# Performance work log

Hardware: AMD Instinct MI355X
Metric: run time of the kernel (lower is better)

Reference implementation:

```python
import jax, jax.numpy as jnp
import numpy as np

E = 600000
N = 50000
H = 128
OE = 256


def swish(v):
    return v * jax.nn.sigmoid(v)


def setup_inputs() -> dict:
    key = jax.random.key(0)
    ks = jax.random.split(key, 16)
    inp = {
        "x": jax.random.normal(ks[0], (E, H), dtype=jnp.float32),
        "rbf": jax.random.normal(ks[1], (E, 6), dtype=jnp.float32),
        "i": jax.random.randint(ks[2], (E,), 0, N, dtype=jnp.int32),
        "edge_index": jax.random.randint(ks[3], (2, E), 0, N, dtype=jnp.int32),
        "edge_weight": jax.random.uniform(ks[4], (E,), dtype=jnp.float32),
        "batch": jax.random.randint(ks[5], (N,), 0, 32, dtype=jnp.int32),
        "num_nodes": N,
        "W_rbf": jax.random.normal(ks[6], (H, 6), dtype=jnp.float32) * 0.2,
        "W_up": jax.random.normal(ks[7], (OE, H), dtype=jnp.float32) * (1.0 / np.sqrt(H)),
        "b_up": jnp.zeros((OE,), dtype=jnp.float32),
        "W_l1": jax.random.normal(ks[8], (OE, OE), dtype=jnp.float32) * (1.0 / np.sqrt(OE)),
        "b_l1": jnp.zeros((OE,), dtype=jnp.float32),
        "W_l2": jax.random.normal(ks[9], (OE, OE), dtype=jnp.float32) * (1.0 / np.sqrt(OE)),
        "b_l2": jnp.zeros((OE,), dtype=jnp.float32),
        "W_l3": jax.random.normal(ks[10], (OE, OE), dtype=jnp.float32) * (1.0 / np.sqrt(OE)),
        "b_l3": jnp.zeros((OE,), dtype=jnp.float32),
        "W_out": jax.random.normal(ks[11], (1, OE), dtype=jnp.float32) * (1.0 / np.sqrt(OE)),
        "W_w": jax.random.normal(ks[12], (1, H), dtype=jnp.float32) * (1.0 / np.sqrt(H)),
        "b_w": jnp.zeros((1,), dtype=jnp.float32),
    }
    return inp


def reference(x, rbf, i, edge_index, edge_weight, batch, num_nodes,
              W_rbf, W_up, b_up, W_l1, b_l1, W_l2, b_l2, W_l3, b_l3,
              W_out, W_w, b_w):
    # edge_index / edge_weight are unused in the original forward.
    # x = lin_rbf(rbf) * x  -> [E, H]
    xe = (rbf @ W_rbf.T) * x
    # scatter-add edges -> nodes: [N, H]
    xn = jax.ops.segment_sum(xe, i, num_segments=num_nodes)
    # energy head: alpha = w_lin(x) before lin_up
    alpha = xn @ W_w.T + b_w  # [N, 1]
    x2 = xn @ W_up.T + b_up   # [N, OE]
    for W, b in ((W_l1, b_l1), (W_l2, b_l2), (W_l3, b_l3)):
        x2 = swish(x2 @ W.T + b)
    out = (x2 @ W_out.T) * alpha  # [N, 1]
    return (out, batch)
```

## Files before the change

kernel.cpp:

```cpp
#include <hip/hip_runtime.h>
#include <hip/hip_bf16.h>
#include <math.h>

#define E_CNT 600000
#define N_CNT 50000
#define H_DIM 128
#define OE_DIM 256

typedef __attribute__((ext_vector_type(8))) short short8;
typedef __attribute__((ext_vector_type(4))) float f32x4;

#define WS_EIDS   0
#define WS_OFF    2400000
#define WS_CURS   2600008
#define WS_CNT    2800008
#define WS_WUP    3000016
#define WS_WL1    3065552
#define WS_WL2    3196624
#define WS_WL3    3327696
#define WS_TEXC   3500000
#define WS_BSUM   3700704
#define WS_BEXC   3701728

#define SCAN_NB 196
#define WCONV_NB 896

__global__ __launch_bounds__(256) void histwconv_kernel(
    const int* __restrict__ nid, int* __restrict__ counts,
    const float* __restrict__ Wup, const float* __restrict__ Wl1,
    const float* __restrict__ Wl2, const float* __restrict__ Wl3,
    ushort* __restrict__ dUp, ushort* __restrict__ dL1,
    ushort* __restrict__ dL2, ushort* __restrict__ dL3)
{
    if (blockIdx.x < WCONV_NB) {
        int d = blockIdx.x * 256 + threadIdx.x;
        const float* W;
        ushort* dst;
        int K;
        if (d < 32768)       { W = Wup; dst = dUp; K = 128; }
        else if (d < 98304)  { d -= 32768;  W = Wl1; dst = dL1; K = 256; }
        else if (d < 163840) { d -= 98304;  W = Wl2; dst = dL2; K = 256; }
        else                 { d -= 163840; W = Wl3; dst = dL3; K = 256; }
        int j = d & 7;
        int l = (d >> 3) & 63;
        int KS = K >> 5;
        int ks = (d >> 9) % KS;
        int ot = (d >> 9) / KS;
        int k = ks * 32 + ((l >> 4) << 3) + j;
        int o = ot * 16 + (l & 15);
        __hip_bfloat16 h = __float2bfloat16(W[o * K + k]);
        dst[d] = *(const ushort*)&h;
    } else {
        int nb = gridDim.x - WCONV_NB;
        for (int e = (blockIdx.x - WCONV_NB) * 256 + threadIdx.x; e < E_CNT;
             e += nb * 256)
            atomicAdd(&counts[nid[e]], 1);
    }
}

__global__ __launch_bounds__(256) void scanA_kernel(const int* __restrict__ counts,
                                                    int* __restrict__ texc,
                                                    int* __restrict__ bsum)
{
    __shared__ int s[256];
    const int t = threadIdx.x;
    const int i = blockIdx.x * 256 + t;
    int v = (i < N_CNT) ? counts[i] : 0;
    s[t] = v;
    __syncthreads();
    for (int off = 1; off < 256; off <<= 1) {
        int u = (t >= off) ? s[t - off] : 0;
        __syncthreads();
        s[t] += u;
        __syncthreads();
    }
    texc[i] = s[t] - v;
    if (t == 255) bsum[blockIdx.x] = s[255];
}

__global__ __launch_bounds__(256) void scanB_kernel(const int* __restrict__ bsum,
                                                    int* __restrict__ bexc)
{
    __shared__ int s[256];
    const int t = threadIdx.x;
    int v = (t < SCAN_NB) ? bsum[t] : 0;
    s[t] = v;
    __syncthreads();
    for (int off = 1; off < 256; off <<= 1) {
        int u = (t >= off) ? s[t - off] : 0;
        __syncthreads();
        s[t] += u;
        __syncthreads();
    }
    bexc[t] = s[t] - v;
}

__global__ __launch_bounds__(256) void scanC_kernel(const int* __restrict__ texc,
                                                    const int* __restrict__ bexc,
                                                    int* __restrict__ offs,
                                                    int* __restrict__ cursor)
{
    const int i = blockIdx.x * 256 + threadIdx.x;
    if (i < N_CNT) {
        int o = texc[i] + bexc[i >> 8];
        offs[i] = o;
        cursor[i] = o;
    }
    if (i == 0) offs[N_CNT] = E_CNT;
}

__global__ __launch_bounds__(256) void fill_kernel(const int* __restrict__ nid,
                                                   int* __restrict__ cursor,
                                                   int* __restrict__ eids)
{
    for (int e = blockIdx.x * 256 + threadIdx.x; e < E_CNT; e += gridDim.x * 256) {
        int slot = atomicAdd(&cursor[nid[e]], 1);
        eids[slot] = e;
    }
}

#define MB 64
#define PITCH 264
#define EMAX 2048

template<int KS, bool SW>
__device__ __forceinline__ void layer(const ushort* __restrict__ Wsh,
                                      const float* __restrict__ bias,
                                      const ushort* in_s, ushort* out_s, int tid)
{
    const int w = tid >> 6, lane = tid & 63;
    const int l15 = lane & 15, lg = lane >> 4;

    f32x4 acc[4][2];
#pragma unroll
    for (int mi = 0; mi < 4; ++mi)
#pragma unroll
        for (int oi = 0; oi < 2; ++oi)
            acc[mi][oi] = (f32x4){0.f, 0.f, 0.f, 0.f};

#pragma unroll
    for (int ks = 0; ks < KS; ++ks) {
        short8 b[2];
#pragma unroll
        for (int oi = 0; oi < 2; ++oi)
            b[oi] = *(const short8*)(Wsh + (size_t)(((w * 2 + oi) * KS + ks) * 64 + lane) * 8);
#pragma unroll
        for (int mi = 0; mi < 4; ++mi) {
            short8 a = *(const short8*)(in_s + (mi * 16 + l15) * PITCH + ks * 32 + lg * 8);
#pragma unroll
            for (int oi = 0; oi < 2; ++oi)
                acc[mi][oi] = __builtin_amdgcn_mfma_f32_16x16x32_bf16(a, b[oi], acc[mi][oi], 0, 0, 0);
        }
    }

#pragma unroll
    for (int oi = 0; oi < 2; ++oi) {
        float bv = bias[(w * 2 + oi) * 16 + l15];
#pragma unroll
        for (int mi = 0; mi < 4; ++mi)
#pragma unroll
            for (int r = 0; r < 4; ++r) {
                float v = acc[mi][oi][r] + bv;
                if (SW) v = v / (1.f + __expf(-v));
                __hip_bfloat16 h = __float2bfloat16(v);
                out_s[(mi * 16 + lg * 4 + r) * PITCH + (w * 2 + oi) * 16 + l15] =
                    *(const ushort*)&h;
            }
    }
}

__global__ __launch_bounds__(512, 4) void fused_kernel(
    const float* __restrict__ x, const float* __restrict__ rbf,
    const int* __restrict__ offs, const int* __restrict__ eids,
    const float* __restrict__ W_rbf, const float* __restrict__ W_w,
    const float* __restrict__ b_w,
    const ushort* __restrict__ Wup, const ushort* __restrict__ Wl1,
    const ushort* __restrict__ Wl2, const ushort* __restrict__ Wl3,
    const float* __restrict__ b_up, const float* __restrict__ b_l1,
    const float* __restrict__ b_l2, const float* __restrict__ b_l3,
    const float* __restrict__ W_out, const int* __restrict__ batch,
    float* __restrict__ out)
{
    __shared__ ushort sA[MB * PITCH];
    __shared__ ushort sB[MB * PITCH];
    __shared__ float s_alpha[MB];
    __shared__ int s_eids[EMAX];

    const int tid = threadIdx.x;
    const int w = tid >> 6, lane = tid & 63;
    const int node0 = blockIdx.x * MB;

    if (tid < MB) {
        int node = node0 + tid;
        if (node < N_CNT) out[N_CNT + node] = (float)batch[node];
    }

    const int nend = min(node0 + MB, N_CNT);
    const int s0 = offs[node0];
    const int tot = offs[nend] - s0;
    const bool staged = (tot <= EMAX);
    if (staged)
        for (int t = tid; t < tot; t += 512) s_eids[t] = eids[s0 + t];
    const int* ep = staged ? (const int*)s_eids : (eids + s0);
    __syncthreads();

    {
        const int half = lane >> 5;
        const int hb = (lane & 31) * 4;
        float wrb[4][6];
#pragma unroll
        for (int j = 0; j < 4; ++j)
#pragma unroll
            for (int k = 0; k < 6; ++k)
                wrb[j][k] = W_rbf[(hb + j) * 6 + k];
        float ww[4];
#pragma unroll
        for (int j = 0; j < 4; ++j) ww[j] = W_w[hb + j];

        for (int nl8 = 0; nl8 < 8; ++nl8) {
            const int nl = w * 8 + nl8;
            const int node = node0 + nl;
            int ls = 0, le = 0;
            if (node < N_CNT) {
                ls = offs[node] - s0;
                le = offs[node + 1] - s0;
            }
            float a0 = 0.f, a1 = 0.f, a2 = 0.f, a3 = 0.f;
            int i = ls;
            for (; i + 1 < le; i += 2) {
                const int ee = ep[i + half];
                const float4 xv = *(const float4*)(x + (size_t)ee * H_DIM + hb);
                float r[6];
#pragma unroll
                for (int k = 0; k < 6; ++k) r[k] = rbf[ee * 6 + k];
                float c0 = 0.f, c1 = 0.f, c2 = 0.f, c3 = 0.f;
#pragma unroll
                for (int k = 0; k < 6; ++k) {
                    c0 = fmaf(r[k], wrb[0][k], c0);
                    c1 = fmaf(r[k], wrb[1][k], c1);
                    c2 = fmaf(r[k], wrb[2][k], c2);
                    c3 = fmaf(r[k], wrb[3][k], c3);
                }
                a0 = fmaf(c0, xv.x, a0);
                a1 = fmaf(c1, xv.y, a1);
                a2 = fmaf(c2, xv.z, a2);
                a3 = fmaf(c3, xv.w, a3);
            }
            if (i < le && half == 0) {
                const int ee = ep[i];
                const float4 xv = *(const float4*)(x + (size_t)ee * H_DIM + hb);
                float r[6];
#pragma unroll
                for (int k = 0; k < 6; ++k) r[k] = rbf[ee * 6 + k];
                float c0 = 0.f, c1 = 0.f, c2 = 0.f, c3 = 0.f;
#pragma unroll
                for (int k = 0; k < 6; ++k) {
                    c0 = fmaf(r[k], wrb[0][k], c0);
                    c1 = fmaf(r[k], wrb[1][k], c1);
                    c2 = fmaf(r[k], wrb[2][k], c2);
                    c3 = fmaf(r[k], wrb[3][k], c3);
                }
                a0 = fmaf(c0, xv.x, a0);
                a1 = fmaf(c1, xv.y, a1);
                a2 = fmaf(c2, xv.z, a2);
                a3 = fmaf(c3, xv.w, a3);
            }

            a0 += __shfl_xor(a0, 32);
            a1 += __shfl_xor(a1, 32);
            a2 += __shfl_xor(a2, 32);
            a3 += __shfl_xor(a3, 32);

            if (half == 0) {
                __hip_bfloat16 h0 = __float2bfloat16(a0), h1 = __float2bfloat16(a1);
                __hip_bfloat16 h2 = __float2bfloat16(a2), h3 = __float2bfloat16(a3);
                ushort4 pk;
                pk.x = *(const ushort*)&h0;
                pk.y = *(const ushort*)&h1;
                pk.z = *(const ushort*)&h2;
                pk.w = *(const ushort*)&h3;
                *(ushort4*)(sA + nl * PITCH + hb) = pk;
            }

            float part = fmaf(a0, ww[0], fmaf(a1, ww[1], fmaf(a2, ww[2], a3 * ww[3])));
            part += __shfl_xor(part, 1);
            part += __shfl_xor(part, 2);
            part += __shfl_xor(part, 4);
            part += __shfl_xor(part, 8);
            part += __shfl_xor(part, 16);
            if (lane == 0) s_alpha[nl] = part + b_w[0];
        }
    }
    __syncthreads();

    layer<4, false>(Wup, b_up, sA, sB, tid);
    __syncthreads();
    layer<8, true>(Wl1, b_l1, sB, sA, tid);
    __syncthreads();
    layer<8, true>(Wl2, b_l2, sA, sB, tid);
    __syncthreads();
    layer<8, true>(Wl3, b_l3, sB, sA, tid);
    __syncthreads();

    {
        int nl = tid >> 3, q = tid & 7;
        const ushort* rowp = sA + nl * PITCH + q * 32;
        float sum = 0.f;
#pragma unroll
        for (int o = 0; o < 32; ++o) {
            __hip_bfloat16 h = *(const __hip_bfloat16*)(rowp + o);
            sum = fmaf(__bfloat162float(h), W_out[q * 32 + o], sum);
        }
        sum += __shfl_xor(sum, 1);
        sum += __shfl_xor(sum, 2);
        sum += __shfl_xor(sum, 4);
        int node = node0 + nl;
        if (q == 0 && node < N_CNT) out[node] = sum * s_alpha[nl];
    }
}

extern "C" void kernel_launch(void* const* d_in, const int* in_sizes, int n_in,
                              void* d_out, int out_size, void* d_ws, size_t ws_size,
                              hipStream_t stream)
{
    const float* x      = (const float*)d_in[0];
    const float* rbf    = (const float*)d_in[1];
    const int*   nid    = (const int*)d_in[2];
    const int*   batch  = (const int*)d_in[5];
    const float* W_rbf  = (const float*)d_in[7];
    const float* W_up   = (const float*)d_in[8];
    const float* b_up   = (const float*)d_in[9];
    const float* W_l1   = (const float*)d_in[10];
    const float* b_l1   = (const float*)d_in[11];
    const float* W_l2   = (const float*)d_in[12];
    const float* b_l2   = (const float*)d_in[13];
    const float* W_l3   = (const float*)d_in[14];
    const float* b_l3   = (const float*)d_in[15];
    const float* W_out  = (const float*)d_in[16];
    const float* W_w    = (const float*)d_in[17];
    const float* b_w    = (const float*)d_in[18];

    char* ws = (char*)d_ws;
    int*    eids   = (int*)(ws + WS_EIDS);
    int*    offs   = (int*)(ws + WS_OFF);
    int*    cursor = (int*)(ws + WS_CURS);
    int*    counts = (int*)(ws + WS_CNT);
    ushort* WupS   = (ushort*)(ws + WS_WUP);
    ushort* Wl1S   = (ushort*)(ws + WS_WL1);
    ushort* Wl2S   = (ushort*)(ws + WS_WL2);
    ushort* Wl3S   = (ushort*)(ws + WS_WL3);
    int*    texc   = (int*)(ws + WS_TEXC);
    int*    bsum   = (int*)(ws + WS_BSUM);
    int*    bexc   = (int*)(ws + WS_BEXC);
    float*  out    = (float*)d_out;

    hipMemsetAsync(counts, 0, N_CNT * sizeof(int), stream);
    histwconv_kernel<<<WCONV_NB + 1024, 256, 0, stream>>>(
        nid, counts, W_up, W_l1, W_l2, W_l3, WupS, Wl1S, Wl2S, Wl3S);
    scanA_kernel<<<SCAN_NB, 256, 0, stream>>>(counts, texc, bsum);
    scanB_kernel<<<1, 256, 0, stream>>>(bsum, bexc);
    scanC_kernel<<<SCAN_NB, 256, 0, stream>>>(texc, bexc, offs, cursor);
    fill_kernel<<<1024, 256, 0, stream>>>(nid, cursor, eids);

    fused_kernel<<<(N_CNT + MB - 1) / MB, 512, 0, stream>>>(
        x, rbf, offs, eids, W_rbf, W_w, b_w,
        WupS, Wl1S, Wl2S, Wl3S, b_up, b_l1, b_l2, b_l3, W_out, batch, out);
}
```

Measured before the change: 226.7 us.

## Single-buffer activations in LDS and raise occupancy of fused node kernel

```diff
diff --git a/kernel.cpp b/kernel.cpp
--- a/kernel.cpp
+++ b/kernel.cpp
@@ -121,12 +121,93 @@
 
 #define MB 64
 #define PITCH 264
-#define EMAX 2048
+#define EMAX 1280
+
+__device__ __forceinline__ void gather_phase(
+    const int* ep,
+    const float* __restrict__ x, const float* __restrict__ rbf,
+    const int* s_off, int s0, float bw,
+    const float (&wrb)[4][6], const float (&ww)[4],
+    ushort* act, float* s_alpha, int w, int lane)
+{
+    const int half = lane >> 5;
+    const int hb = (lane & 31) * 4;
+
+    for (int nl8 = 0; nl8 < 8; ++nl8) {
+        const int nl = w * 8 + nl8;
+        const int ls = s_off[nl] - s0;
+        const int le = s_off[nl + 1] - s0;
+        float a0 = 0.f, a1 = 0.f, a2 = 0.f, a3 = 0.f;
+        int i = ls;
+        for (; i + 1 < le; i += 2) {
+            const int ee = ep[i + half];
+            const float4 xv = *(const float4*)(x + (size_t)ee * H_DIM + hb);
+            const float2* rp = (const float2*)(rbf + (size_t)ee * 6);
+            const float2 r01 = rp[0], r23 = rp[1], r45 = rp[2];
+            float r[6] = {r01.x, r01.y, r23.x, r23.y, r45.x, r45.y};
+            float c0 = 0.f, c1 = 0.f, c2 = 0.f, c3 = 0.f;
+#pragma unroll
+            for (int k = 0; k < 6; ++k) {
+                c0 = fmaf(r[k], wrb[0][k], c0);
+                c1 = fmaf(r[k], wrb[1][k], c1);
+                c2 = fmaf(r[k], wrb[2][k], c2);
+                c3 = fmaf(r[k], wrb[3][k], c3);
+            }
+            a0 = fmaf(c0, xv.x, a0);
+            a1 = fmaf(c1, xv.y, a1);
+            a2 = fmaf(c2, xv.z, a2);
+            a3 = fmaf(c3, xv.w, a3);
+        }
+        if (i < le && half == 0) {
+            const int ee = ep[i];
+            const float4 xv = *(const float4*)(x + (size_t)ee * H_DIM + hb);
+            const float2* rp = (const float2*)(rbf + (size_t)ee * 6);
+            const float2 r01 = rp[0], r23 = rp[1], r45 = rp[2];
+            float r[6] = {r01.x, r01.y, r23.x, r23.y, r45.x, r45.y};
+            float c0 = 0.f, c1 = 0.f, c2 = 0.f, c3 = 0.f;
+#pragma unroll
+            for (int k = 0; k < 6; ++k) {
+                c0 = fmaf(r[k], wrb[0][k], c0);
+                c1 = fmaf(r[k], wrb[1][k], c1);
+                c2 = fmaf(r[k], wrb[2][k], c2);
+                c3 = fmaf(r[k], wrb[3][k], c3);
+            }
+            a0 = fmaf(c0, xv.x, a0);
+            a1 = fmaf(c1, xv.y, a1);
+            a2 = fmaf(c2, xv.z, a2);
+            a3 = fmaf(c3, xv.w, a3);
+        }
+
+        a0 += __shfl_xor(a0, 32);
+        a1 += __shfl_xor(a1, 32);
+        a2 += __shfl_xor(a2, 32);
+        a3 += __shfl_xor(a3, 32);
+
+        if (half == 0) {
+            __hip_bfloat16 h0 = __float2bfloat16(a0), h1 = __float2bfloat16(a1);
+            __hip_bfloat16 h2 = __float2bfloat16(a2), h3 = __float2bfloat16(a3);
+            ushort4 pk;
+            pk.x = *(const ushort*)&h0;
+            pk.y = *(const ushort*)&h1;
+            pk.z = *(const ushort*)&h2;
+            pk.w = *(const ushort*)&h3;
+            *(ushort4*)(act + nl * PITCH + hb) = pk;
+        }
+
+        float part = fmaf(a0, ww[0], fmaf(a1, ww[1], fmaf(a2, ww[2], a3 * ww[3])));
+        part += __shfl_xor(part, 1);
+        part += __shfl_xor(part, 2);
+        part += __shfl_xor(part, 4);
+        part += __shfl_xor(part, 8);
+        part += __shfl_xor(part, 16);
+        if (lane == 0) s_alpha[nl] = part + bw;
+    }
+}
 
 template<int KS, bool SW>
-__device__ __forceinline__ void layer(const ushort* __restrict__ Wsh,
-                                      const float* __restrict__ bias,
-                                      const ushort* in_s, ushort* out_s, int tid)
+__device__ __forceinline__ void layer_sb(const ushort* __restrict__ Wsh,
+                                         const float* __restrict__ bias,
+                                         ushort* act, int tid)
 {
     const int w = tid >> 6, lane = tid & 63;
     const int l15 = lane & 15, lg = lane >> 4;
@@ -146,12 +227,13 @@
             b[oi] = *(const short8*)(Wsh + (size_t)(((w * 2 + oi) * KS + ks) * 64 + lane) * 8);
 #pragma unroll
         for (int mi = 0; mi < 4; ++mi) {
-            short8 a = *(const short8*)(in_s + (mi * 16 + l15) * PITCH + ks * 32 + lg * 8);
+            short8 a = *(const short8*)(act + (mi * 16 + l15) * PITCH + ks * 32 + lg * 8);
 #pragma unroll
             for (int oi = 0; oi < 2; ++oi)
                 acc[mi][oi] = __builtin_amdgcn_mfma_f32_16x16x32_bf16(a, b[oi], acc[mi][oi], 0, 0, 0);
         }
     }
+    __syncthreads();
 
 #pragma unroll
     for (int oi = 0; oi < 2; ++oi) {
@@ -163,13 +245,14 @@
                 float v = acc[mi][oi][r] + bv;
                 if (SW) v = v / (1.f + __expf(-v));
                 __hip_bfloat16 h = __float2bfloat16(v);
-                out_s[(mi * 16 + lg * 4 + r) * PITCH + (w * 2 + oi) * 16 + l15] =
+                act[(mi * 16 + lg * 4 + r) * PITCH + (w * 2 + oi) * 16 + l15] =
                     *(const ushort*)&h;
             }
     }
-}
-
-__global__ __launch_bounds__(512, 4) void fused_kernel(
+    __syncthreads();
+}
+
+__global__ __launch_bounds__(512, 8) void fused_kernel(
     const float* __restrict__ x, const float* __restrict__ rbf,
     const int* __restrict__ offs, const int* __restrict__ eids,
     const float* __restrict__ W_rbf, const float* __restrict__ W_w,
@@ -181,10 +264,10 @@
     const float* __restrict__ W_out, const int* __restrict__ batch,
     float* __restrict__ out)
 {
-    __shared__ ushort sA[MB * PITCH];
-    __shared__ ushort sB[MB * PITCH];
+    __shared__ ushort act[MB * PITCH];
+    __shared__ int s_eids[EMAX];
+    __shared__ int s_off[MB + 1];
     __shared__ float s_alpha[MB];
-    __shared__ int s_eids[EMAX];
 
     const int tid = threadIdx.x;
     const int w = tid >> 6, lane = tid & 63;
@@ -194,18 +277,18 @@
         int node = node0 + tid;
         if (node < N_CNT) out[N_CNT + node] = (float)batch[node];
     }
-
-    const int nend = min(node0 + MB, N_CNT);
-    const int s0 = offs[node0];
-    const int tot = offs[nend] - s0;
+    if (tid < MB + 1)
+        s_off[tid] = offs[min(node0 + tid, N_CNT)];
+    __syncthreads();
+
+    const int s0 = s_off[0];
+    const int tot = s_off[MB] - s0;
     const bool staged = (tot <= EMAX);
     if (staged)
         for (int t = tid; t < tot; t += 512) s_eids[t] = eids[s0 + t];
-    const int* ep = staged ? (const int*)s_eids : (eids + s0);
     __syncthreads();
 
     {
-        const int half = lane >> 5;
         const int hb = (lane & 31) * 4;
         float wrb[4][6];
 #pragma unroll
@@ -216,95 +299,23 @@
         float ww[4];
 #pragma unroll
         for (int j = 0; j < 4; ++j) ww[j] = W_w[hb + j];
-
-        for (int nl8 = 0; nl8 < 8; ++nl8) {
-            const int nl = w * 8 + nl8;
-            const int node = node0 + nl;
-            int ls = 0, le = 0;
-            if (node < N_CNT) {
-                ls = offs[node] - s0;
-                le = offs[node + 1] - s0;
-            }
-            float a0 = 0.f, a1 = 0.f, a2 = 0.f, a3 = 0.f;
-            int i = ls;
-            for (; i + 1 < le; i += 2) {
-                const int ee = ep[i + half];
-                const float4 xv = *(const float4*)(x + (size_t)ee * H_DIM + hb);
-                float r[6];
-#pragma unroll
-                for (int k = 0; k < 6; ++k) r[k] = rbf[ee * 6 + k];
-                float c0 = 0.f, c1 = 0.f, c2 = 0.f, c3 = 0.f;
-#pragma unroll
-                for (int k = 0; k < 6; ++k) {
-                    c0 = fmaf(r[k], wrb[0][k], c0);
-                    c1 = fmaf(r[k], wrb[1][k], c1);
-                    c2 = fmaf(r[k], wrb[2][k], c2);
-                    c3 = fmaf(r[k], wrb[3][k], c3);
-                }
-                a0 = fmaf(c0, xv.x, a0);
-                a1 = fmaf(c1, xv.y, a1);
-                a2 = fmaf(c2, xv.z, a2);
-                a3 = fmaf(c3, xv.w, a3);
-            }
-            if (i < le && half == 0) {
-                const int ee = ep[i];
-                const float4 xv = *(const float4*)(x + (size_t)ee * H_DIM + hb);
-                float r[6];
-#pragma unroll
-                for (int k = 0; k < 6; ++k) r[k] = rbf[ee * 6 + k];
-                float c0 = 0.f, c1 = 0.f, c2 = 0.f, c3 = 0.f;
-#pragma unroll
-                for (int k = 0; k < 6; ++k) {
-                    c0 = fmaf(r[k], wrb[0][k], c0);
-                    c1 = fmaf(r[k], wrb[1][k], c1);
-                    c2 = fmaf(r[k], wrb[2][k], c2);
-                    c3 = fmaf(r[k], wrb[3][k], c3);
-                }
-                a0 = fmaf(c0, xv.x, a0);
-                a1 = fmaf(c1, xv.y, a1);
-                a2 = fmaf(c2, xv.z, a2);
-                a3 = fmaf(c3, xv.w, a3);
-            }
-
-            a0 += __shfl_xor(a0, 32);
-            a1 += __shfl_xor(a1, 32);
-            a2 += __shfl_xor(a2, 32);
-            a3 += __shfl_xor(a3, 32);
-
-            if (half == 0) {
-                __hip_bfloat16 h0 = __float2bfloat16(a0), h1 = __float2bfloat16(a1);
-                __hip_bfloat16 h2 = __float2bfloat16(a2), h3 = __float2bfloat16(a3);
-                ushort4 pk;
-                pk.x = *(const ushort*)&h0;
-                pk.y = *(const ushort*)&h1;
-                pk.z = *(const ushort*)&h2;
-                pk.w = *(const ushort*)&h3;
-                *(ushort4*)(sA + nl * PITCH + hb) = pk;
-            }
-
-            float part = fmaf(a0, ww[0], fmaf(a1, ww[1], fmaf(a2, ww[2], a3 * ww[3])));
-            part += __shfl_xor(part, 1);
-            part += __shfl_xor(part, 2);
-            part += __shfl_xor(part, 4);
-            part += __shfl_xor(part, 8);
-            part += __shfl_xor(part, 16);
-            if (lane == 0) s_alpha[nl] = part + b_w[0];
-        }
-    }
-    __syncthreads();
-
-    layer<4, false>(Wup, b_up, sA, sB, tid);
-    __syncthreads();
-    layer<8, true>(Wl1, b_l1, sB, sA, tid);
-    __syncthreads();
-    layer<8, true>(Wl2, b_l2, sA, sB, tid);
-    __syncthreads();
-    layer<8, true>(Wl3, b_l3, sB, sA, tid);
-    __syncthreads();
+        const float bw = b_w[0];
+
+        if (staged)
+            gather_phase(s_eids, x, rbf, s_off, s0, bw, wrb, ww, act, s_alpha, w, lane);
+        else
+            gather_phase(eids + s0, x, rbf, s_off, s0, bw, wrb, ww, act, s_alpha, w, lane);
+    }
+    __syncthreads();
+
+    layer_sb<4, false>(Wup, b_up, act, tid);
+    layer_sb<8, true>(Wl1, b_l1, act, tid);
+    layer_sb<8, true>(Wl2, b_l2, act, tid);
+    layer_sb<8, true>(Wl3, b_l3, act, tid);
 
     {
         int nl = tid >> 3, q = tid & 7;
-        const ushort* rowp = sA + nl * PITCH + q * 32;
+        const ushort* rowp = act + nl * PITCH + q * 32;
         float sum = 0.f;
 #pragma unroll
         for (int o = 0; o < 32; ++o) {
```

Result: slower. 255.8 us (+12.8%).

## Halve node tile to 32 and stream edge ids through chunked shared staging

Applied to the files above, without the earlier changes.

```diff
diff --git a/kernel.cpp b/kernel.cpp
--- a/kernel.cpp
+++ b/kernel.cpp
@@ -119,9 +119,9 @@
     }
 }
 
-#define MB 64
+#define MB 32
 #define PITCH 264
-#define EMAX 2048
+#define EMAX 640
 
 template<int KS, bool SW>
 __device__ __forceinline__ void layer(const ushort* __restrict__ Wsh,
@@ -131,25 +131,22 @@
     const int w = tid >> 6, lane = tid & 63;
     const int l15 = lane & 15, lg = lane >> 4;
 
-    f32x4 acc[4][2];
-#pragma unroll
-    for (int mi = 0; mi < 4; ++mi)
+    f32x4 acc[2][2];
+#pragma unroll
+    for (int mi = 0; mi < 2; ++mi)
 #pragma unroll
         for (int oi = 0; oi < 2; ++oi)
             acc[mi][oi] = (f32x4){0.f, 0.f, 0.f, 0.f};
 
 #pragma unroll
     for (int ks = 0; ks < KS; ++ks) {
-        short8 b[2];
-#pragma unroll
-        for (int oi = 0; oi < 2; ++oi)
-            b[oi] = *(const short8*)(Wsh + (size_t)(((w * 2 + oi) * KS + ks) * 64 + lane) * 8);
-#pragma unroll
-        for (int mi = 0; mi < 4; ++mi) {
+        short8 b0 = *(const short8*)(Wsh + (size_t)(((w * 2 + 0) * KS + ks) * 64 + lane) * 8);
+        short8 b1 = *(const short8*)(Wsh + (size_t)(((w * 2 + 1) * KS + ks) * 64 + lane) * 8);
+#pragma unroll
+        for (int mi = 0; mi < 2; ++mi) {
             short8 a = *(const short8*)(in_s + (mi * 16 + l15) * PITCH + ks * 32 + lg * 8);
-#pragma unroll
-            for (int oi = 0; oi < 2; ++oi)
-                acc[mi][oi] = __builtin_amdgcn_mfma_f32_16x16x32_bf16(a, b[oi], acc[mi][oi], 0, 0, 0);
+            acc[mi][0] = __builtin_amdgcn_mfma_f32_16x16x32_bf16(a, b0, acc[mi][0], 0, 0, 0);
+            acc[mi][1] = __builtin_amdgcn_mfma_f32_16x16x32_bf16(a, b1, acc[mi][1], 0, 0, 0);
         }
     }
 
@@ -157,7 +154,7 @@
     for (int oi = 0; oi < 2; ++oi) {
         float bv = bias[(w * 2 + oi) * 16 + l15];
 #pragma unroll
-        for (int mi = 0; mi < 4; ++mi)
+        for (int mi = 0; mi < 2; ++mi)
 #pragma unroll
             for (int r = 0; r < 4; ++r) {
                 float v = acc[mi][oi][r] + bv;
@@ -169,7 +166,7 @@
     }
 }
 
-__global__ __launch_bounds__(512, 4) void fused_kernel(
+__global__ __launch_bounds__(512, 8) void fused_kernel(
     const float* __restrict__ x, const float* __restrict__ rbf,
     const int* __restrict__ offs, const int* __restrict__ eids,
     const float* __restrict__ W_rbf, const float* __restrict__ W_w,
@@ -183,8 +180,9 @@
 {
     __shared__ ushort sA[MB * PITCH];
     __shared__ ushort sB[MB * PITCH];
+    __shared__ int s_eids[EMAX];
+    __shared__ int s_off[MB + 1];
     __shared__ float s_alpha[MB];
-    __shared__ int s_eids[EMAX];
 
     const int tid = threadIdx.x;
     const int w = tid >> 6, lane = tid & 63;
@@ -194,15 +192,13 @@
         int node = node0 + tid;
         if (node < N_CNT) out[N_CNT + node] = (float)batch[node];
     }
-
-    const int nend = min(node0 + MB, N_CNT);
-    const int s0 = offs[node0];
-    const int tot = offs[nend] - s0;
-    const bool staged = (tot <= EMAX);
-    if (staged)
-        for (int t = tid; t < tot; t += 512) s_eids[t] = eids[s0 + t];
-    const int* ep = staged ? (const int*)s_eids : (eids + s0);
-    __syncthreads();
+    if (tid < MB + 1)
+        s_off[tid] = offs[min(node0 + tid, N_CNT)];
+    __syncthreads();
+
+    const int s0 = s_off[0];
+    const int tot = s_off[MB] - s0;
+    const int nchunks = (tot + EMAX - 1) / EMAX;
 
     {
         const int half = lane >> 5;
@@ -216,79 +212,95 @@
         float ww[4];
 #pragma unroll
         for (int j = 0; j < 4; ++j) ww[j] = W_w[hb + j];
-
-        for (int nl8 = 0; nl8 < 8; ++nl8) {
-            const int nl = w * 8 + nl8;
-            const int node = node0 + nl;
-            int ls = 0, le = 0;
-            if (node < N_CNT) {
-                ls = offs[node] - s0;
-                le = offs[node + 1] - s0;
+        const float bw = b_w[0];
+
+        for (int c = 0; c < nchunks; ++c) {
+            const int cs = c * EMAX;
+            const int ce = min(cs + EMAX, tot);
+            __syncthreads();
+            for (int t = tid + cs; t < ce; t += 512) s_eids[t - cs] = eids[s0 + t];
+            __syncthreads();
+
+            for (int nl4 = 0; nl4 < 4; ++nl4) {
+                const int nl = (w << 2) + nl4;
+                const int ls = max(s_off[nl] - s0, cs);
+                const int le = min(s_off[nl + 1] - s0, ce);
+                float a0 = 0.f, a1 = 0.f, a2 = 0.f, a3 = 0.f;
+                int i = ls;
+                for (; i + 1 < le; i += 2) {
+                    const int ee = s_eids[i - cs + half];
+                    const float4 xv = *(const float4*)(x + (size_t)ee * H_DIM + hb);
+                    const float2* rp = (const float2*)(rbf + (size_t)ee * 6);
+                    const float2 r01 = rp[0], r23 = rp[1], r45 = rp[2];
+                    float r[6] = {r01.x, r01.y, r23.x, r23.y, r45.x, r45.y};
+                    float c0 = 0.f, c1 = 0.f, c2 = 0.f, c3 = 0.f;
+#pragma unroll
+                    for (int k = 0; k < 6; ++k) {
+                        c0 = fmaf(r[k], wrb[0][k], c0);
+                        c1 = fmaf(r[k], wrb[1][k], c1);
+                        c2 = fmaf(r[k], wrb[2][k], c2);
+                        c3 = fmaf(r[k], wrb[3][k], c3);
+                    }
+                    a0 = fmaf(c0, xv.x, a0);
+                    a1 = fmaf(c1, xv.y, a1);
+                    a2 = fmaf(c2, xv.z, a2);
+                    a3 = fmaf(c3, xv.w, a3);
+                }
+                if (i < le && half == 0) {
+                    const int ee = s_eids[i - cs];
+                    const float4 xv = *(const float4*)(x + (size_t)ee * H_DIM + hb);
+                    const float2* rp = (const float2*)(rbf + (size_t)ee * 6);
+                    const float2 r01 = rp[0], r23 = rp[1], r45 = rp[2];
+                    float r[6] = {r01.x, r01.y, r23.x, r23.y, r45.x, r45.y};
+                    float c0 = 0.f, c1 = 0.f, c2 = 0.f, c3 = 0.f;
+#pragma unroll
+                    for (int k = 0; k < 6; ++k) {
+                        c0 = fmaf(r[k], wrb[0][k], c0);
+                        c1 = fmaf(r[k], wrb[1][k], c1);
+                        c2 = fmaf(r[k], wrb[2][k], c2);
+                        c3 = fmaf(r[k], wrb[3][k], c3);
+                    }
+                    a0 = fmaf(c0, xv.x, a0);
+                    a1 = fmaf(c1, xv.y, a1);
+                    a2 = fmaf(c2, xv.z, a2);
+                    a3 = fmaf(c3, xv.w, a3);
+                }
+
+                a0 += __shfl_xor(a0, 32);
+                a1 += __shfl_xor(a1, 32);
+                a2 += __shfl_xor(a2, 32);
+                a3 += __shfl_xor(a3, 32);
+
+                if (half == 0) {
+                    ushort4* dp = (ushort4*)(sA + nl * PITCH + hb);
+                    if (c > 0) {
+                        ushort4 old = *dp;
+                        a0 += __bfloat162float(*(const __hip_bfloat16*)&old.x);
+                        a1 += __bfloat162float(*(const __hip_bfloat16*)&old.y);
+                        a2 += __bfloat162float(*(const __hip_bfloat16*)&old.z);
+                        a3 += __bfloat162float(*(const __hip_bfloat16*)&old.w);
+                    }
+                    __hip_bfloat16 h0 = __float2bfloat16(a0), h1 = __float2bfloat16(a1);
+                    __hip_bfloat16 h2 = __float2bfloat16(a2), h3 = __float2bfloat16(a3);
+                    ushort4 pk;
+                    pk.x = *(const ushort*)&h0;
+                    pk.y = *(const ushort*)&h1;
+                    pk.z = *(const ushort*)&h2;
+                    pk.w = *(const ushort*)&h3;
+                    *dp = pk;
+                }
+
+                float part = fmaf(a0, ww[0], fmaf(a1, ww[1], fmaf(a2, ww[2], a3 * ww[3])));
+                part += __shfl_xor(part, 1);
+                part += __shfl_xor(part, 2);
+                part += __shfl_xor(part, 4);
+                part += __shfl_xor(part, 8);
+                part += __shfl_xor(part, 16);
+                if (lane == 0) {
+                    if (c > 0) s_alpha[nl] += part;
+                    else       s_alpha[nl] = part + bw;
+                }
             }
-            float a0 = 0.f, a1 = 0.f, a2 = 0.f, a3 = 0.f;
-            int i = ls;
-            for (; i + 1 < le; i += 2) {
-                const int ee = ep[i + half];
-                const float4 xv = *(const float4*)(x + (size_t)ee * H_DIM + hb);
-                float r[6];
-#pragma unroll
-                for (int k = 0; k < 6; ++k) r[k] = rbf[ee * 6 + k];
-                float c0 = 0.f, c1 = 0.f, c2 = 0.f, c3 = 0.f;
-#pragma unroll
-                for (int k = 0; k < 6; ++k) {
-                    c0 = fmaf(r[k], wrb[0][k], c0);
-                    c1 = fmaf(r[k], wrb[1][k], c1);
-                    c2 = fmaf(r[k], wrb[2][k], c2);
-                    c3 = fmaf(r[k], wrb[3][k], c3);
-                }
-                a0 = fmaf(c0, xv.x, a0);
-                a1 = fmaf(c1, xv.y, a1);
-                a2 = fmaf(c2, xv.z, a2);
-                a3 = fmaf(c3, xv.w, a3);
-            }
-            if (i < le && half == 0) {
-                const int ee = ep[i];
-                const float4 xv = *(const float4*)(x + (size_t)ee * H_DIM + hb);
-                float r[6];
-#pragma unroll
-                for (int k = 0; k < 6; ++k) r[k] = rbf[ee * 6 + k];
-                float c0 = 0.f, c1 = 0.f, c2 = 0.f, c3 = 0.f;
-#pragma unroll
-                for (int k = 0; k < 6; ++k) {
-                    c0 = fmaf(r[k], wrb[0][k], c0);
-                    c1 = fmaf(r[k], wrb[1][k], c1);
-                    c2 = fmaf(r[k], wrb[2][k], c2);
-                    c3 = fmaf(r[k], wrb[3][k], c3);
-                }
-                a0 = fmaf(c0, xv.x, a0);
-                a1 = fmaf(c1, xv.y, a1);
-                a2 = fmaf(c2, xv.z, a2);
-                a3 = fmaf(c3, xv.w, a3);
-            }
-
-            a0 += __shfl_xor(a0, 32);
-            a1 += __shfl_xor(a1, 32);
-            a2 += __shfl_xor(a2, 32);
-            a3 += __shfl_xor(a3, 32);
-
-            if (half == 0) {
-                __hip_bfloat16 h0 = __float2bfloat16(a0), h1 = __float2bfloat16(a1);
-                __hip_bfloat16 h2 = __float2bfloat16(a2), h3 = __float2bfloat16(a3);
-                ushort4 pk;
-                pk.x = *(const ushort*)&h0;
-                pk.y = *(const ushort*)&h1;
-                pk.z = *(const ushort*)&h2;
-                pk.w = *(const ushort*)&h3;
-                *(ushort4*)(sA + nl * PITCH + hb) = pk;
-            }
-
-            float part = fmaf(a0, ww[0], fmaf(a1, ww[1], fmaf(a2, ww[2], a3 * ww[3])));
-            part += __shfl_xor(part, 1);
-            part += __shfl_xor(part, 2);
-            part += __shfl_xor(part, 4);
-            part += __shfl_xor(part, 8);
-            part += __shfl_xor(part, 16);
-            if (lane == 0) s_alpha[nl] = part + b_w[0];
         }
     }
     __syncthreads();
@@ -303,17 +315,18 @@
     __syncthreads();
 
     {
-        int nl = tid >> 3, q = tid & 7;
-        const ushort* rowp = sA + nl * PITCH + q * 32;
+        int nl = tid >> 4, q = tid & 15;
+        const ushort* rowp = sA + nl * PITCH + q * 16;
         float sum = 0.f;
 #pragma unroll
-        for (int o = 0; o < 32; ++o) {
+        for (int o = 0; o < 16; ++o) {
             __hip_bfloat16 h = *(const __hip_bfloat16*)(rowp + o);
-            sum = fmaf(__bfloat162float(h), W_out[q * 32 + o], sum);
+            sum = fmaf(__bfloat162float(h), W_out[q * 16 + o], sum);
         }
         sum += __shfl_xor(sum, 1);
         sum += __shfl_xor(sum, 2);
         sum += __shfl_xor(sum, 4);
+        sum += __shfl_xor(sum, 8);
         int node = node0 + nl;
         if (q == 0 && node < N_CNT) out[node] = sum * s_alpha[nl];
     }
```

Measured after the change: 223.6 us. No clear change (-1.3%).
